# Kernel tuning notes

Hardware: AMD Instinct MI355X
Metric: run time of the kernel (lower is better)

## Reference

```python
import jax, jax.numpy as jnp
import numpy as np

B, H, S, D = 8, 16, 1024, 64

def setup_inputs() -> dict:
    key = jax.random.key(0)
    kq, kk, kv, km = jax.random.split(key, 4)
    Q = jax.random.normal(kq, (B, H, S, D), dtype=jnp.float32)
    K = jax.random.normal(kk, (B, H, S, D), dtype=jnp.float32)
    V = jax.random.normal(kv, (B, H, S, D), dtype=jnp.float32)
    attn_mask = jax.random.randint(km, (B, H, S, S), 0, 2).astype(bool)
    return {"Q": Q, "K": K, "V": V, "attn_mask": attn_mask}

def reference(Q, K, V, attn_mask):
    # scores = Q @ K^T  (NOTE: source has no 1/sqrt(d) scaling)
    scores = jnp.einsum("bhqd,bhkd->bhqk", Q, K)
    # source uses masked_fill_(mask, 1e-9), i.e. masked positions become 1e-9 (not -inf)
    scores = jnp.where(attn_mask, jnp.float32(1e-9), scores)
    attn = jax.nn.softmax(scores, axis=-1)
    context = jnp.einsum("bhqk,bhkd->bhqd", attn, V)
    return context, attn
```

## Files before the change

kernel.cpp:

```cpp
#include <hip/hip_runtime.h>

#define Sn 1024
#define Dn 64
#define PH_LD 1032
#define K_LD 72
#define V_LD 72

typedef short v8s __attribute__((ext_vector_type(8)));
typedef unsigned short v8u __attribute__((ext_vector_type(8)));
typedef float v4f __attribute__((ext_vector_type(4)));
typedef int   v4i __attribute__((ext_vector_type(4)));

#define LGKM0()  asm volatile("s_waitcnt lgkmcnt(0)" ::: "memory")
#define SBAR()   do { asm volatile("" ::: "memory"); __builtin_amdgcn_s_barrier(); \
                      __builtin_amdgcn_sched_barrier(0); } while (0)

__device__ __forceinline__ unsigned short f2bf(float x) {
    union { float f; unsigned u; } v; v.f = x;
    return (unsigned short)((v.u + 0x7FFFu + ((v.u >> 16) & 1u)) >> 16);
}
__device__ __forceinline__ float bf2f(unsigned short h) {
    union { float f; unsigned u; } v; v.u = ((unsigned)h) << 16;
    return v.f;
}
__device__ __forceinline__ void split2(float x, unsigned short& h, unsigned short& l) {
    unsigned short hs = f2bf(x);
    h = hs; l = f2bf(x - bf2f(hs));
}

__global__ __launch_bounds__(256) void prep_all(
    const float* __restrict__ K, const float* __restrict__ V,
    const int* __restrict__ M,
    unsigned short* __restrict__ KF, unsigned short* __restrict__ VF,
    unsigned long long* __restrict__ MW)
{
    __shared__ float Ts[64][65];
    const int bid = blockIdx.x;
    const int t = threadIdx.x;

    if (bid < 2048) {
        const int bh = bid >> 4, kt = bid & 15;
        const int w = t >> 6, lane = t & 63;
        const int fr = lane & 15, g = lane >> 4;
        const float* src = K + (((size_t)(bh << 10) + (kt << 6) + (w << 4) + fr) << 6);
        const v4f a0 = __builtin_nontemporal_load((const v4f*)(src + (g << 3)));
        const v4f a1 = __builtin_nontemporal_load((const v4f*)(src + (g << 3) + 4));
        const v4f b0 = __builtin_nontemporal_load((const v4f*)(src + 32 + (g << 3)));
        const v4f b1 = __builtin_nontemporal_load((const v4f*)(src + 32 + (g << 3) + 4));
        v8u h0, h1, l0, l1;
        #pragma unroll
        for (int j = 0; j < 4; ++j) {
            unsigned short hh, ll;
            split2(a0[j], hh, ll); h0[j] = hh;     l0[j] = ll;
            split2(a1[j], hh, ll); h0[4 + j] = hh; l0[4 + j] = ll;
            split2(b0[j], hh, ll); h1[j] = hh;     l1[j] = ll;
            split2(b1[j], hh, ll); h1[4 + j] = hh; l1[4 + j] = ll;
        }
        unsigned short* dst = KF + ((size_t)bh << 17) + ((size_t)((kt << 2) + w) << 11) + (lane << 3);
        *(v8u*)(dst)        = h0;
        *(v8u*)(dst + 512)  = h1;
        *(v8u*)(dst + 1024) = l0;
        *(v8u*)(dst + 1536) = l1;
    } else if (bid < 4096) {
        const int b2 = bid - 2048;
        const int bh = b2 >> 4, kt = b2 & 15;
        {
            const int r = t >> 2, cs = (t & 3) << 4;
            const float* src = V + ((size_t)bh * Sn + (kt << 6) + r) * Dn + cs;
            const v4f a = __builtin_nontemporal_load((const v4f*)src);
            const v4f b = __builtin_nontemporal_load((const v4f*)src + 1);
            const v4f c = __builtin_nontemporal_load((const v4f*)src + 2);
            const v4f d = __builtin_nontemporal_load((const v4f*)src + 3);
            #pragma unroll
            for (int j = 0; j < 4; ++j) {
                Ts[r][cs + j]      = a[j];
                Ts[r][cs + 4 + j]  = b[j];
                Ts[r][cs + 8 + j]  = c[j];
                Ts[r][cs + 12 + j] = d[j];
            }
        }
        __syncthreads();
        {
            const int w = t >> 6, lane = t & 63;
            const int fr = lane & 15, g = lane >> 4;
            const int d = (w << 4) + fr;
            unsigned short* dst = VF + ((size_t)bh << 16) + ((size_t)((kt << 2) + w) << 10) + (lane << 3);
            v8u o0, o1;
            #pragma unroll
            for (int j = 0; j < 8; ++j) o0[j] = f2bf(Ts[(g << 3) + j][d]);
            #pragma unroll
            for (int j = 0; j < 8; ++j) o1[j] = f2bf(Ts[32 + (g << 3) + j][d]);
            *(v8u*)dst         = o0;
            *(v8u*)(dst + 512) = o1;
        }
    } else {
        const int NW = 2097152;
        const int lane = t & 63;
        const int wave = ((bid - 4096) << 2) + (t >> 6);
        const int nwaves = 2048 << 2;
        for (int w0 = wave << 3; w0 < NW; w0 += nwaves << 3) {
            unsigned long long b[8];
            #pragma unroll
            for (int s = 0; s < 8; ++s) {
                const int v = __builtin_nontemporal_load(&M[((size_t)(w0 + s) << 6) + lane]);
                b[s] = __ballot(v != 0);
            }
            if (lane == 0) {
                ulonglong2* dst = (ulonglong2*)(MW + w0);
                ulonglong2 p0, p1, p2, p3;
                p0.x = b[0]; p0.y = b[1]; p1.x = b[2]; p1.y = b[3];
                p2.x = b[4]; p2.y = b[5]; p3.x = b[6]; p3.y = b[7];
                dst[0] = p0; dst[1] = p1; dst[2] = p2; dst[3] = p3;
            }
        }
    }
}

__global__ __launch_bounds__(256, 4) void fused_attn_c(
    const unsigned short* __restrict__ KFG, const unsigned short* __restrict__ VFG,
    const float* __restrict__ Q, const unsigned long long* __restrict__ MW,
    float* __restrict__ attnO, float* __restrict__ ctxO)
{
    __shared__ unsigned short Ph[16][PH_LD];
    __shared__ float rsumW[4][16];
    __shared__ float invL[16];

    const int tid  = threadIdx.x;
    const int lane = tid & 63;
    const int w    = tid >> 6;
    const int fr   = lane & 15;
    const int g    = lane >> 4;

    const int swz = ((blockIdx.x & 7) << 10) + (blockIdx.x >> 3);
    const int bh = swz >> 6;
    const int q0 = (swz & 63) << 4;

    const float* Qb = Q + (size_t)bh * Sn * Dn + (size_t)q0 * Dn;
    float*       Ab = attnO + (size_t)bh * Sn * Sn + (size_t)q0 * Sn;
    float*       Cb = ctxO  + (size_t)bh * Sn * Dn + (size_t)q0 * Dn;
    const unsigned short* KFb = KFG + ((size_t)bh << 17);
    const unsigned short* VFb = VFG + ((size_t)bh << 16);
    const unsigned long long* mwp = MW + ((size_t)bh << 14) + ((size_t)(q0 + fr) << 4);

    v8s qh0, qh1, ql0, ql1;
    {
        const float* qp = Qb + fr * Dn + (g << 3);
        float x0[8], x1[8];
        *(v4f*)&x0[0] = *(const v4f*)qp;
        *(v4f*)&x0[4] = *(const v4f*)(qp + 4);
        *(v4f*)&x1[0] = *(const v4f*)(qp + 32);
        *(v4f*)&x1[4] = *(const v4f*)(qp + 36);
        #pragma unroll
        for (int i = 0; i < 8; ++i) {
            unsigned short hh, ll;
            split2(x0[i], hh, ll); qh0[i] = (short)hh; ql0[i] = (short)ll;
            split2(x1[i], hh, ll); qh1[i] = (short)hh; ql1[i] = (short)ll;
        }
    }

    const int sh = (w << 4) + (g << 2);

#define LDK(kt, h0_, h1_, l0_, l1_) do {                                           \
        const unsigned short* _p = KFb + ((size_t)(((kt) << 2) + w) << 11) + (lane << 3); \
        h0_ = *(const v8s*)_p;          h1_ = *(const v8s*)(_p + 512);             \
        l0_ = *(const v8s*)(_p + 1024); l1_ = *(const v8s*)(_p + 1536);            \
    } while (0)

#define STEPA(h0_, h1_, l0_, l1_, mwv, kt) do {                                    \
        v4f acc = {0.f, 0.f, 0.f, 0.f};                                            \
        __builtin_amdgcn_s_setprio(1);                                             \
        acc = __builtin_amdgcn_mfma_f32_16x16x32_bf16(h0_, qh0, acc, 0, 0, 0);     \
        acc = __builtin_amdgcn_mfma_f32_16x16x32_bf16(h1_, qh1, acc, 0, 0, 0);     \
        acc = __builtin_amdgcn_mfma_f32_16x16x32_bf16(l0_, qh0, acc, 0, 0, 0);     \
        acc = __builtin_amdgcn_mfma_f32_16x16x32_bf16(l1_, qh1, acc, 0, 0, 0);     \
        acc = __builtin_amdgcn_mfma_f32_16x16x32_bf16(h0_, ql0, acc, 0, 0, 0);     \
        acc = __builtin_amdgcn_mfma_f32_16x16x32_bf16(h1_, ql1, acc, 0, 0, 0);     \
        __builtin_amdgcn_s_setprio(0);                                             \
        const unsigned mb = (unsigned)((mwv) >> sh);                               \
        const float e0 = (mb & 1u) ? 1.0f : __expf(acc[0]);                        \
        const float e1 = (mb & 2u) ? 1.0f : __expf(acc[1]);                        \
        const float e2 = (mb & 4u) ? 1.0f : __expf(acc[2]);                        \
        const float e3 = (mb & 8u) ? 1.0f : __expf(acc[3]);                        \
        rs += (e0 + e1) + (e2 + e3);                                               \
        ushort4 pk;                                                                \
        pk.x = f2bf(e0); pk.y = f2bf(e1); pk.z = f2bf(e2); pk.w = f2bf(e3);        \
        *(ushort4*)&Ph[fr][((kt) << 6) + (w << 4) + (g << 2)] = pk;                \
    } while (0)

    float rs = 0.f;

    {
        v8s h0[4], h1[4], l0[4], l1[4];
        unsigned long long mk[4];
        LDK(0, h0[0], h1[0], l0[0], l1[0]);
        LDK(1, h0[1], h1[1], l0[1], l1[1]);
        LDK(2, h0[2], h1[2], l0[2], l1[2]);
        LDK(3, h0[3], h1[3], l0[3], l1[3]);
        mk[0] = mwp[0]; mk[1] = mwp[1]; mk[2] = mwp[2]; mk[3] = mwp[3];
        #pragma unroll
        for (int kt = 0; kt < 16; ++kt) {
            STEPA(h0[kt & 3], h1[kt & 3], l0[kt & 3], l1[kt & 3], mk[kt & 3], kt);
            if (kt + 4 < 16) {
                LDK(kt + 4, h0[kt & 3], h1[kt & 3], l0[kt & 3], l1[kt & 3]);
                mk[kt & 3] = mwp[kt + 4];
            }
        }
    }

    rs += __shfl_xor(rs, 16);
    rs += __shfl_xor(rs, 32);
    if (g == 0) rsumW[w][fr] = rs;
    __builtin_amdgcn_sched_barrier(0);
    LGKM0();
    SBAR();
    if (tid < 16) {
        const float s = rsumW[0][tid] + rsumW[1][tid] + rsumW[2][tid] + rsumW[3][tid];
        invL[tid] = 1.0f / s;
    }
    __builtin_amdgcn_sched_barrier(0);
    LGKM0();
    SBAR();

#define LDV(kt, v0_, v1_) do {                                                     \
        const unsigned short* _p = VFb + ((size_t)(((kt) << 2) + w) << 10) + (lane << 3); \
        v0_ = *(const v8s*)_p;  v1_ = *(const v8s*)(_p + 512);                     \
    } while (0)

#define STEPB(v0_, v1_, kt) do {                                                   \
        const v8s a0 = *(const v8s*)&Ph[fr][((kt) << 6) + (g << 3)];               \
        const v8s a1 = *(const v8s*)&Ph[fr][((kt) << 6) + 32 + (g << 3)];          \
        __builtin_amdgcn_s_setprio(1);                                             \
        accp = __builtin_amdgcn_mfma_f32_16x16x32_bf16(a0, v0_, accp, 0, 0, 0);    \
        accp = __builtin_amdgcn_mfma_f32_16x16x32_bf16(a1, v1_, accp, 0, 0, 0);    \
        __builtin_amdgcn_s_setprio(0);                                             \
    } while (0)

    v8s v0s[4], v1s[4];
    LDV(0, v0s[0], v1s[0]);
    LDV(1, v0s[1], v1s[1]);
    LDV(2, v0s[2], v1s[2]);
    LDV(3, v0s[3], v1s[3]);

    {
        const int qq = tid >> 4, ii = tid & 15;
        const float inv = invL[qq];
        float* arow = Ab + (size_t)qq * Sn;
        #pragma unroll
        for (int c = 0; c < 16; ++c) {
            const int k0 = (c << 6) + (ii << 2);
            const ushort4 p = *(const ushort4*)&Ph[qq][k0];
            v4f o;
            o[0] = bf2f(p.x) * inv; o[1] = bf2f(p.y) * inv;
            o[2] = bf2f(p.z) * inv; o[3] = bf2f(p.w) * inv;
            __builtin_nontemporal_store(o, (v4f*)(arow + k0));
        }
    }

    const int dcol = (w << 4) + fr;
    v4f accp = {0.f, 0.f, 0.f, 0.f};
    #pragma unroll
    for (int kt = 0; kt < 16; ++kt) {
        STEPB(v0s[kt & 3], v1s[kt & 3], kt);
        if (kt + 4 < 16) LDV(kt + 4, v0s[kt & 3], v1s[kt & 3]);
    }
    #pragma unroll
    for (int r = 0; r < 4; ++r) {
        const int q = (g << 2) + r;
        __builtin_nontemporal_store(accp[r] * invL[q], &Cb[(size_t)q * Dn + dcol]);
    }
#undef LDK
#undef STEPA
#undef LDV
#undef STEPB
}

__global__ __launch_bounds__(256, 3) void fused_attn_fb(
    const float* __restrict__ Q, const float* __restrict__ K,
    const float* __restrict__ V, const int* __restrict__ M,
    float* __restrict__ attnO, float* __restrict__ ctxO)
{
    __shared__ unsigned short Ph[16][1048];
    __shared__ __align__(16) unsigned short Kraw[2 * 64 * K_LD];
    __shared__ float rsumW[4][16];
    __shared__ float invL[16];

    unsigned short (*Khi)[K_LD] = (unsigned short (*)[K_LD])Kraw;
    unsigned short (*Klo)[K_LD] = (unsigned short (*)[K_LD])(Kraw + 64 * K_LD);
    unsigned short (*Vt)[V_LD]  = (unsigned short (*)[V_LD])Kraw;

    const int tid  = threadIdx.x;
    const int lane = tid & 63;
    const int w    = tid >> 6;
    const int fr   = lane & 15;
    const int g    = lane >> 4;

    const int bh = blockIdx.x >> 6;
    const int q0 = (blockIdx.x & 63) << 4;

    const float* Qb = Q + (size_t)bh * Sn * Dn + (size_t)q0 * Dn;
    const float* Kb = K + (size_t)bh * Sn * Dn;
    const float* Vb = V + (size_t)bh * Sn * Dn;
    const int*   Mb = M + (size_t)bh * Sn * Sn + (size_t)q0 * Sn;
    float*       Ab = attnO + (size_t)bh * Sn * Sn + (size_t)q0 * Sn;
    float*       Cb = ctxO  + (size_t)bh * Sn * Dn + (size_t)q0 * Dn;

    v8s qh0, qh1, ql0, ql1;
    {
        const float* qp = Qb + fr * Dn + (g << 3);
        float x0[8], x1[8];
        *(v4f*)&x0[0] = *(const v4f*)qp;
        *(v4f*)&x0[4] = *(const v4f*)(qp + 4);
        *(v4f*)&x1[0] = *(const v4f*)(qp + 32);
        *(v4f*)&x1[4] = *(const v4f*)(qp + 36);
        #pragma unroll
        for (int i = 0; i < 8; ++i) {
            unsigned short hh, ll;
            split2(x0[i], hh, ll); qh0[i] = (short)hh; ql0[i] = (short)ll;
            split2(x1[i], hh, ll); qh1[i] = (short)hh; ql1[i] = (short)ll;
        }
    }

    const int srow = tid >> 4;
    const int sc4  = (tid & 15) << 2;

    const int* mp = Mb + (size_t)fr * Sn + (w << 4) + (g << 2);
    v4i mv = *(const v4i*)mp;

    v4f ka[4];
    #pragma unroll
    for (int i = 0; i < 4; ++i)
        ka[i] = *(const v4f*)(Kb + (size_t)(srow + (i << 4)) * Dn + sc4);

    float rs = 0.f;

    for (int kt = 0; kt < 16; ++kt) {
        __syncthreads();
        v4f kb[4];
        if (kt < 15) {
            const float* kn = Kb + (size_t)((kt + 1) << 6) * Dn;
            #pragma unroll
            for (int i = 0; i < 4; ++i)
                kb[i] = *(const v4f*)(kn + (size_t)(srow + (i << 4)) * Dn + sc4);
        }
        v4i mnext = mv;
        if (kt < 15) mnext = *(const v4i*)(mp + ((kt + 1) << 6));

        #pragma unroll
        for (int i = 0; i < 4; ++i) {
            const int row = srow + (i << 4);
            ushort4 hv, lv;
            split2(ka[i][0], hv.x, lv.x); split2(ka[i][1], hv.y, lv.y);
            split2(ka[i][2], hv.z, lv.z); split2(ka[i][3], hv.w, lv.w);
            *(ushort4*)&Khi[row][sc4] = hv;
            *(ushort4*)&Klo[row][sc4] = lv;
        }
        __syncthreads();

        const int krow = (w << 4) + fr;
        const v8s kh0 = *(const v8s*)&Khi[krow][(g << 3)];
        const v8s kh1 = *(const v8s*)&Khi[krow][32 + (g << 3)];
        const v8s kl0 = *(const v8s*)&Klo[krow][(g << 3)];
        const v8s kl1 = *(const v8s*)&Klo[krow][32 + (g << 3)];

        v4f acc = {0.f, 0.f, 0.f, 0.f};
        acc = __builtin_amdgcn_mfma_f32_16x16x32_bf16(kh0, qh0, acc, 0, 0, 0);
        acc = __builtin_amdgcn_mfma_f32_16x16x32_bf16(kh1, qh1, acc, 0, 0, 0);
        acc = __builtin_amdgcn_mfma_f32_16x16x32_bf16(kl0, qh0, acc, 0, 0, 0);
        acc = __builtin_amdgcn_mfma_f32_16x16x32_bf16(kl1, qh1, acc, 0, 0, 0);
        acc = __builtin_amdgcn_mfma_f32_16x16x32_bf16(kh0, ql0, acc, 0, 0, 0);
        acc = __builtin_amdgcn_mfma_f32_16x16x32_bf16(kh1, ql1, acc, 0, 0, 0);

        const float e0 = mv[0] ? 1.0f : __expf(acc[0]);
        const float e1 = mv[1] ? 1.0f : __expf(acc[1]);
        const float e2 = mv[2] ? 1.0f : __expf(acc[2]);
        const float e3 = mv[3] ? 1.0f : __expf(acc[3]);
        rs += (e0 + e1) + (e2 + e3);
        ushort4 pk;
        pk.x = f2bf(e0); pk.y = f2bf(e1); pk.z = f2bf(e2); pk.w = f2bf(e3);
        *(ushort4*)&Ph[fr][(kt << 6) + (w << 4) + (g << 2)] = pk;

        mv = mnext;
        #pragma unroll
        for (int i = 0; i < 4; ++i) ka[i] = kb[i];
    }

    rs += __shfl_xor(rs, 16);
    rs += __shfl_xor(rs, 32);
    if (g == 0) rsumW[w][fr] = rs;
    __syncthreads();
    if (tid < 16) {
        const float s = rsumW[0][tid] + rsumW[1][tid] + rsumW[2][tid] + rsumW[3][tid];
        invL[tid] = 1.0f / s;
    }
    __syncthreads();

    const int dcol = (w << 4) + fr;
    v4f va[4];
    #pragma unroll
    for (int i = 0; i < 4; ++i)
        va[i] = *(const v4f*)(Vb + (size_t)(srow + (i << 4)) * Dn + sc4);

    v4f accp = {0.f, 0.f, 0.f, 0.f};
    for (int kt = 0; kt < 16; ++kt) {
        __syncthreads();
        v4f vb[4];
        if (kt < 15) {
            const float* vn = Vb + (size_t)((kt + 1) << 6) * Dn;
            #pragma unroll
            for (int i = 0; i < 4; ++i)
                vb[i] = *(const v4f*)(vn + (size_t)(srow + (i << 4)) * Dn + sc4);
        }
        #pragma unroll
        for (int i = 0; i < 4; ++i) {
            const int row = srow + (i << 4);
            Vt[sc4 + 0][row] = f2bf(va[i][0]);
            Vt[sc4 + 1][row] = f2bf(va[i][1]);
            Vt[sc4 + 2][row] = f2bf(va[i][2]);
            Vt[sc4 + 3][row] = f2bf(va[i][3]);
        }
        __syncthreads();

        #pragma unroll
        for (int c = 0; c < 2; ++c) {
            const int kc = (kt << 6) + (c << 5);
            const v8s a = *(const v8s*)&Ph[fr][kc + (g << 3)];
            const v8s b = *(const v8s*)&Vt[dcol][(c << 5) + (g << 3)];
            accp = __builtin_amdgcn_mfma_f32_16x16x32_bf16(a, b, accp, 0, 0, 0);
        }
        #pragma unroll
        for (int i = 0; i < 4; ++i) va[i] = vb[i];
    }
    #pragma unroll
    for (int r = 0; r < 4; ++r) {
        const int q = (g << 2) + r;
        Cb[(size_t)q * Dn + dcol] = accp[r] * invL[q];
    }

    {
        const int qq = tid >> 4, ii = tid & 15;
        const float inv = invL[qq];
        float* arow = Ab + (size_t)qq * Sn;
        #pragma unroll
        for (int c = 0; c < 16; ++c) {
            const int k0 = (c << 6) + (ii << 2);
            const ushort4 p = *(const ushort4*)&Ph[qq][k0];
            v4f o;
            o[0] = bf2f(p.x) * inv; o[1] = bf2f(p.y) * inv;
            o[2] = bf2f(p.z) * inv; o[3] = bf2f(p.w) * inv;
            *(v4f*)(arow + k0) = o;
        }
    }
}

extern "C" void kernel_launch(void* const* d_in, const int* in_sizes, int n_in,
                              void* d_out, int out_size, void* d_ws, size_t ws_size,
                              hipStream_t stream) {
    const float* Q    = (const float*)d_in[0];
    const float* K    = (const float*)d_in[1];
    const float* V    = (const float*)d_in[2];
    const int*   mask = (const int*)d_in[3];

    float* ctx  = (float*)d_out;
    float* attn = (float*)d_out + (size_t)128 * Sn * Dn;

    const size_t NELEM = (size_t)128 * Sn * Dn;
    const size_t MWORDS = (size_t)128 * Sn * 16;
    const size_t NEED  = NELEM * 6 + MWORDS * 8;

    if (ws_size >= NEED) {
        unsigned short* KF = (unsigned short*)d_ws;
        unsigned short* VF = KF + NELEM * 2;
        unsigned long long* MWp = (unsigned long long*)((char*)d_ws + NELEM * 6);
        prep_all<<<6144, 256, 0, stream>>>(K, V, mask, KF, VF, MWp);
        fused_attn_c<<<128 * 64, 256, 0, stream>>>(KF, VF, Q, MWp, attn, ctx);
    } else {
        fused_attn_fb<<<128 * 64, 256, 0, stream>>>(Q, K, V, mask, attn, ctx);
    }
}
```

Baseline: 301.2 us.

## Double attention block to 512 threads with split-K PV reduction; split prep kernel

The main attention kernel now uses 8 waves per 16-query block instead of 4. Each wave computes half as many QK^T key slices, and the PV product is split across two key halves whose partial sums are combined through shared memory. The combined prep kernel is also split into three separate launches for K, V and the mask bitpacking. The aim is more wave-level parallelism and latency hiding per block. The cost is an extra barrier and shared-memory reduction, plus two more kernel launches.

Result: faster. 295.2 us (-2.0%).

```diff
diff --git a/kernel.cpp b/kernel.cpp
--- a/kernel.cpp
+++ b/kernel.cpp
@@ -28,102 +28,104 @@
     h = hs; l = f2bf(x - bf2f(hs));
 }
 
-__global__ __launch_bounds__(256) void prep_all(
-    const float* __restrict__ K, const float* __restrict__ V,
-    const int* __restrict__ M,
-    unsigned short* __restrict__ KF, unsigned short* __restrict__ VF,
+__global__ __launch_bounds__(256) void prep_kf(const float* __restrict__ K,
+    unsigned short* __restrict__ KF)
+{
+    const int bh = blockIdx.x >> 4, kt = blockIdx.x & 15;
+    const int t = threadIdx.x;
+    const int w = t >> 6, lane = t & 63;
+    const int fr = lane & 15, g = lane >> 4;
+    const float* src = K + (((size_t)(bh << 10) + (kt << 6) + (w << 4) + fr) << 6);
+    const v4f a0 = __builtin_nontemporal_load((const v4f*)(src + (g << 3)));
+    const v4f a1 = __builtin_nontemporal_load((const v4f*)(src + (g << 3) + 4));
+    const v4f b0 = __builtin_nontemporal_load((const v4f*)(src + 32 + (g << 3)));
+    const v4f b1 = __builtin_nontemporal_load((const v4f*)(src + 32 + (g << 3) + 4));
+    v8u h0, h1, l0, l1;
+    #pragma unroll
+    for (int j = 0; j < 4; ++j) {
+        unsigned short hh, ll;
+        split2(a0[j], hh, ll); h0[j] = hh;     l0[j] = ll;
+        split2(a1[j], hh, ll); h0[4 + j] = hh; l0[4 + j] = ll;
+        split2(b0[j], hh, ll); h1[j] = hh;     l1[j] = ll;
+        split2(b1[j], hh, ll); h1[4 + j] = hh; l1[4 + j] = ll;
+    }
+    unsigned short* dst = KF + ((size_t)bh << 17) + ((size_t)((kt << 2) + w) << 11) + (lane << 3);
+    *(v8u*)(dst)        = h0;
+    *(v8u*)(dst + 512)  = h1;
+    *(v8u*)(dst + 1024) = l0;
+    *(v8u*)(dst + 1536) = l1;
+}
+
+__global__ __launch_bounds__(256) void prep_vf(const float* __restrict__ V,
+    unsigned short* __restrict__ VF)
+{
+    __shared__ float Ts[64][65];
+    const int bh = blockIdx.x >> 4, kt = blockIdx.x & 15;
+    const int t = threadIdx.x;
+    {
+        const int r = t >> 2, cs = (t & 3) << 4;
+        const float* src = V + ((size_t)bh * Sn + (kt << 6) + r) * Dn + cs;
+        const v4f a = __builtin_nontemporal_load((const v4f*)src);
+        const v4f b = __builtin_nontemporal_load((const v4f*)src + 1);
+        const v4f c = __builtin_nontemporal_load((const v4f*)src + 2);
+        const v4f d = __builtin_nontemporal_load((const v4f*)src + 3);
+        #pragma unroll
+        for (int j = 0; j < 4; ++j) {
+            Ts[r][cs + j]      = a[j];
+            Ts[r][cs + 4 + j]  = b[j];
+            Ts[r][cs + 8 + j]  = c[j];
+            Ts[r][cs + 12 + j] = d[j];
+        }
+    }
+    __syncthreads();
+    {
+        const int w = t >> 6, lane = t & 63;
+        const int fr = lane & 15, g = lane >> 4;
+        const int d = (w << 4) + fr;
+        unsigned short* dst = VF + ((size_t)bh << 16) + ((size_t)((kt << 2) + w) << 10) + (lane << 3);
+        v8u o0, o1;
+        #pragma unroll
+        for (int j = 0; j < 8; ++j) o0[j] = f2bf(Ts[(g << 3) + j][d]);
+        #pragma unroll
+        for (int j = 0; j < 8; ++j) o1[j] = f2bf(Ts[32 + (g << 3) + j][d]);
+        *(v8u*)dst         = o0;
+        *(v8u*)(dst + 512) = o1;
+    }
+}
+
+__global__ __launch_bounds__(256) void prep_m(const int* __restrict__ M,
     unsigned long long* __restrict__ MW)
 {
-    __shared__ float Ts[64][65];
-    const int bid = blockIdx.x;
-    const int t = threadIdx.x;
-
-    if (bid < 2048) {
-        const int bh = bid >> 4, kt = bid & 15;
-        const int w = t >> 6, lane = t & 63;
-        const int fr = lane & 15, g = lane >> 4;
-        const float* src = K + (((size_t)(bh << 10) + (kt << 6) + (w << 4) + fr) << 6);
-        const v4f a0 = __builtin_nontemporal_load((const v4f*)(src + (g << 3)));
-        const v4f a1 = __builtin_nontemporal_load((const v4f*)(src + (g << 3) + 4));
-        const v4f b0 = __builtin_nontemporal_load((const v4f*)(src + 32 + (g << 3)));
-        const v4f b1 = __builtin_nontemporal_load((const v4f*)(src + 32 + (g << 3) + 4));
-        v8u h0, h1, l0, l1;
-        #pragma unroll
-        for (int j = 0; j < 4; ++j) {
-            unsigned short hh, ll;
-            split2(a0[j], hh, ll); h0[j] = hh;     l0[j] = ll;
-            split2(a1[j], hh, ll); h0[4 + j] = hh; l0[4 + j] = ll;
-            split2(b0[j], hh, ll); h1[j] = hh;     l1[j] = ll;
-            split2(b1[j], hh, ll); h1[4 + j] = hh; l1[4 + j] = ll;
-        }
-        unsigned short* dst = KF + ((size_t)bh << 17) + ((size_t)((kt << 2) + w) << 11) + (lane << 3);
-        *(v8u*)(dst)        = h0;
-        *(v8u*)(dst + 512)  = h1;
-        *(v8u*)(dst + 1024) = l0;
-        *(v8u*)(dst + 1536) = l1;
-    } else if (bid < 4096) {
-        const int b2 = bid - 2048;
-        const int bh = b2 >> 4, kt = b2 & 15;
-        {
-            const int r = t >> 2, cs = (t & 3) << 4;
-            const float* src = V + ((size_t)bh * Sn + (kt << 6) + r) * Dn + cs;
-            const v4f a = __builtin_nontemporal_load((const v4f*)src);
-            const v4f b = __builtin_nontemporal_load((const v4f*)src + 1);
-            const v4f c = __builtin_nontemporal_load((const v4f*)src + 2);
-            const v4f d = __builtin_nontemporal_load((const v4f*)src + 3);
-            #pragma unroll
-            for (int j = 0; j < 4; ++j) {
-                Ts[r][cs + j]      = a[j];
-                Ts[r][cs + 4 + j]  = b[j];
-                Ts[r][cs + 8 + j]  = c[j];
-                Ts[r][cs + 12 + j] = d[j];
-            }
-        }
-        __syncthreads();
-        {
-            const int w = t >> 6, lane = t & 63;
-            const int fr = lane & 15, g = lane >> 4;
-            const int d = (w << 4) + fr;
-            unsigned short* dst = VF + ((size_t)bh << 16) + ((size_t)((kt << 2) + w) << 10) + (lane << 3);
-            v8u o0, o1;
-            #pragma unroll
-            for (int j = 0; j < 8; ++j) o0[j] = f2bf(Ts[(g << 3) + j][d]);
-            #pragma unroll
-            for (int j = 0; j < 8; ++j) o1[j] = f2bf(Ts[32 + (g << 3) + j][d]);
-            *(v8u*)dst         = o0;
-            *(v8u*)(dst + 512) = o1;
-        }
-    } else {
-        const int NW = 2097152;
-        const int lane = t & 63;
-        const int wave = ((bid - 4096) << 2) + (t >> 6);
-        const int nwaves = 2048 << 2;
-        for (int w0 = wave << 3; w0 < NW; w0 += nwaves << 3) {
-            unsigned long long b[8];
-            #pragma unroll
-            for (int s = 0; s < 8; ++s) {
-                const int v = __builtin_nontemporal_load(&M[((size_t)(w0 + s) << 6) + lane]);
-                b[s] = __ballot(v != 0);
-            }
-            if (lane == 0) {
-                ulonglong2* dst = (ulonglong2*)(MW + w0);
-                ulonglong2 p0, p1, p2, p3;
-                p0.x = b[0]; p0.y = b[1]; p1.x = b[2]; p1.y = b[3];
-                p2.x = b[4]; p2.y = b[5]; p3.x = b[6]; p3.y = b[7];
-                dst[0] = p0; dst[1] = p1; dst[2] = p2; dst[3] = p3;
-            }
-        }
-    }
-}
-
-__global__ __launch_bounds__(256, 4) void fused_attn_c(
+    const int NW = 2097152;
+    const int lane = threadIdx.x & 63;
+    const int wave = (blockIdx.x << 2) + (threadIdx.x >> 6);
+    const int nwaves = gridDim.x << 2;
+    for (int w0 = wave << 3; w0 < NW; w0 += nwaves << 3) {
+        unsigned long long b[8];
+        #pragma unroll
+        for (int s = 0; s < 8; ++s) {
+            const int v = __builtin_nontemporal_load(&M[((size_t)(w0 + s) << 6) + lane]);
+            b[s] = __ballot(v != 0);
+        }
+        if (lane == 0) {
+            ulonglong2* dst = (ulonglong2*)(MW + w0);
+            ulonglong2 p0, p1, p2, p3;
+            p0.x = b[0]; p0.y = b[1]; p1.x = b[2]; p1.y = b[3];
+            p2.x = b[4]; p2.y = b[5]; p3.x = b[6]; p3.y = b[7];
+            dst[0] = p0; dst[1] = p1; dst[2] = p2; dst[3] = p3;
+        }
+    }
+}
+
+__global__ __launch_bounds__(512, 6) void fused_attn_h(
     const unsigned short* __restrict__ KFG, const unsigned short* __restrict__ VFG,
     const float* __restrict__ Q, const unsigned long long* __restrict__ MW,
     float* __restrict__ attnO, float* __restrict__ ctxO)
 {
     __shared__ unsigned short Ph[16][PH_LD];
-    __shared__ float rsumW[4][16];
+    __shared__ float rsumW[8][16];
     __shared__ float invL[16];
+    __shared__ float pv[4][16][16];
 
     const int tid  = threadIdx.x;
     const int lane = tid & 63;
@@ -158,15 +160,14 @@
         }
     }
 
-    const int sh = (w << 4) + (g << 2);
-
-#define LDK(kt, h0_, h1_, l0_, l1_) do {                                           \
-        const unsigned short* _p = KFb + ((size_t)(((kt) << 2) + w) << 11) + (lane << 3); \
+#define LDKS(s, h0_, h1_, l0_, l1_) do {                                           \
+        const int _kt = (w << 1) + ((s) >> 2);                                     \
+        const unsigned short* _p = KFb + ((size_t)(((_kt) << 2) + ((s) & 3)) << 11) + (lane << 3); \
         h0_ = *(const v8s*)_p;          h1_ = *(const v8s*)(_p + 512);             \
         l0_ = *(const v8s*)(_p + 1024); l1_ = *(const v8s*)(_p + 1536);            \
     } while (0)
 
-#define STEPA(h0_, h1_, l0_, l1_, mwv, kt) do {                                    \
+#define STEPA(h0_, h1_, l0_, l1_, mwv, s) do {                                     \
         v4f acc = {0.f, 0.f, 0.f, 0.f};                                            \
         __builtin_amdgcn_s_setprio(1);                                             \
         acc = __builtin_amdgcn_mfma_f32_16x16x32_bf16(h0_, qh0, acc, 0, 0, 0);     \
@@ -176,7 +177,8 @@
         acc = __builtin_amdgcn_mfma_f32_16x16x32_bf16(h0_, ql0, acc, 0, 0, 0);     \
         acc = __builtin_amdgcn_mfma_f32_16x16x32_bf16(h1_, ql1, acc, 0, 0, 0);     \
         __builtin_amdgcn_s_setprio(0);                                             \
-        const unsigned mb = (unsigned)((mwv) >> sh);                               \
+        const int _sh = (((s) & 3) << 4) + (g << 2);                               \
+        const unsigned mb = (unsigned)((mwv) >> _sh);                              \
         const float e0 = (mb & 1u) ? 1.0f : __expf(acc[0]);                        \
         const float e1 = (mb & 2u) ? 1.0f : __expf(acc[1]);                        \
         const float e2 = (mb & 4u) ? 1.0f : __expf(acc[2]);                        \
@@ -184,26 +186,23 @@
         rs += (e0 + e1) + (e2 + e3);                                               \
         ushort4 pk;                                                                \
         pk.x = f2bf(e0); pk.y = f2bf(e1); pk.z = f2bf(e2); pk.w = f2bf(e3);        \
-        *(ushort4*)&Ph[fr][((kt) << 6) + (w << 4) + (g << 2)] = pk;                \
+        const int _kc = (((w << 1) + ((s) >> 2)) << 6) + (((s) & 3) << 4) + (g << 2); \
+        *(ushort4*)&Ph[fr][_kc] = pk;                                              \
     } while (0)
 
     float rs = 0.f;
 
     {
-        v8s h0[4], h1[4], l0[4], l1[4];
-        unsigned long long mk[4];
-        LDK(0, h0[0], h1[0], l0[0], l1[0]);
-        LDK(1, h0[1], h1[1], l0[1], l1[1]);
-        LDK(2, h0[2], h1[2], l0[2], l1[2]);
-        LDK(3, h0[3], h1[3], l0[3], l1[3]);
-        mk[0] = mwp[0]; mk[1] = mwp[1]; mk[2] = mwp[2]; mk[3] = mwp[3];
-        #pragma unroll
-        for (int kt = 0; kt < 16; ++kt) {
-            STEPA(h0[kt & 3], h1[kt & 3], l0[kt & 3], l1[kt & 3], mk[kt & 3], kt);
-            if (kt + 4 < 16) {
-                LDK(kt + 4, h0[kt & 3], h1[kt & 3], l0[kt & 3], l1[kt & 3]);
-                mk[kt & 3] = mwp[kt + 4];
-            }
+        v8s h0[2], h1[2], l0[2], l1[2];
+        unsigned long long mk[2];
+        LDKS(0, h0[0], h1[0], l0[0], l1[0]);
+        LDKS(1, h0[1], h1[1], l0[1], l1[1]);
+        mk[0] = mwp[(w << 1)];
+        mk[1] = mwp[(w << 1) + 1];
+        #pragma unroll
+        for (int s = 0; s < 8; ++s) {
+            STEPA(h0[s & 1], h1[s & 1], l0[s & 1], l1[s & 1], mk[s >> 2], s);
+            if (s + 2 < 8) LDKS(s + 2, h0[s & 1], h1[s & 1], l0[s & 1], l1[s & 1]);
         }
     }
 
@@ -214,15 +213,22 @@
     LGKM0();
     SBAR();
     if (tid < 16) {
-        const float s = rsumW[0][tid] + rsumW[1][tid] + rsumW[2][tid] + rsumW[3][tid];
+        float s = 0.f;
+        #pragma unroll
+        for (int ww = 0; ww < 8; ++ww) s += rsumW[ww][tid];
         invL[tid] = 1.0f / s;
     }
     __builtin_amdgcn_sched_barrier(0);
     LGKM0();
     SBAR();
 
+    const int dsl  = w & 3;
+    const int half = w >> 2;
+    const int ktb  = half << 3;
+    const int dcol = (dsl << 4) + fr;
+
 #define LDV(kt, v0_, v1_) do {                                                     \
-        const unsigned short* _p = VFb + ((size_t)(((kt) << 2) + w) << 10) + (lane << 3); \
+        const unsigned short* _p = VFb + ((size_t)(((kt) << 2) + dsl) << 10) + (lane << 3); \
         v0_ = *(const v8s*)_p;  v1_ = *(const v8s*)(_p + 512);                     \
     } while (0)
 
@@ -235,19 +241,41 @@
         __builtin_amdgcn_s_setprio(0);                                             \
     } while (0)
 
-    v8s v0s[4], v1s[4];
-    LDV(0, v0s[0], v1s[0]);
-    LDV(1, v0s[1], v1s[1]);
-    LDV(2, v0s[2], v1s[2]);
-    LDV(3, v0s[3], v1s[3]);
-
-    {
-        const int qq = tid >> 4, ii = tid & 15;
+    v4f accp = {0.f, 0.f, 0.f, 0.f};
+    {
+        v8s v0s[2], v1s[2];
+        LDV(ktb + 0, v0s[0], v1s[0]);
+        LDV(ktb + 1, v0s[1], v1s[1]);
+        #pragma unroll
+        for (int i = 0; i < 8; ++i) {
+            STEPB(v0s[i & 1], v1s[i & 1], ktb + i);
+            if (i + 2 < 8) LDV(ktb + i + 2, v0s[i & 1], v1s[i & 1]);
+        }
+    }
+
+    if (half) {
+        #pragma unroll
+        for (int r = 0; r < 4; ++r) pv[dsl][(g << 2) + r][fr] = accp[r];
+    }
+    __builtin_amdgcn_sched_barrier(0);
+    LGKM0();
+    SBAR();
+    if (!half) {
+        #pragma unroll
+        for (int r = 0; r < 4; ++r) {
+            const int q = (g << 2) + r;
+            const float o = (accp[r] + pv[dsl][q][fr]) * invL[q];
+            __builtin_nontemporal_store(o, &Cb[(size_t)q * Dn + dcol]);
+        }
+    }
+
+    {
+        const int qq = tid >> 5, ii = tid & 31;
         const float inv = invL[qq];
         float* arow = Ab + (size_t)qq * Sn;
         #pragma unroll
-        for (int c = 0; c < 16; ++c) {
-            const int k0 = (c << 6) + (ii << 2);
+        for (int c = 0; c < 8; ++c) {
+            const int k0 = (c << 7) + (ii << 2);
             const ushort4 p = *(const ushort4*)&Ph[qq][k0];
             v4f o;
             o[0] = bf2f(p.x) * inv; o[1] = bf2f(p.y) * inv;
@@ -255,20 +283,7 @@
             __builtin_nontemporal_store(o, (v4f*)(arow + k0));
         }
     }
-
-    const int dcol = (w << 4) + fr;
-    v4f accp = {0.f, 0.f, 0.f, 0.f};
-    #pragma unroll
-    for (int kt = 0; kt < 16; ++kt) {
-        STEPB(v0s[kt & 3], v1s[kt & 3], kt);
-        if (kt + 4 < 16) LDV(kt + 4, v0s[kt & 3], v1s[kt & 3]);
-    }
-    #pragma unroll
-    for (int r = 0; r < 4; ++r) {
-        const int q = (g << 2) + r;
-        __builtin_nontemporal_store(accp[r] * invL[q], &Cb[(size_t)q * Dn + dcol]);
-    }
-#undef LDK
+#undef LDKS
 #undef STEPA
 #undef LDV
 #undef STEPB
@@ -471,8 +486,10 @@
         unsigned short* KF = (unsigned short*)d_ws;
         unsigned short* VF = KF + NELEM * 2;
         unsigned long long* MWp = (unsigned long long*)((char*)d_ws + NELEM * 6);
-        prep_all<<<6144, 256, 0, stream>>>(K, V, mask, KF, VF, MWp);
-        fused_attn_c<<<128 * 64, 256, 0, stream>>>(KF, VF, Q, MWp, attn, ctx);
+        prep_kf<<<2048, 256, 0, stream>>>(K, KF);
+        prep_vf<<<2048, 256, 0, stream>>>(V, VF);
+        prep_m<<<2048, 256, 0, stream>>>(mask, MWp);
+        fused_attn_h<<<128 * 64, 512, 0, stream>>>(KF, VF, Q, MWp, attn, ctx);
     } else {
         fused_attn_fb<<<128 * 64, 256, 0, stream>>>(Q, K, V, mask, attn, ctx);
     }
```
